# Performance work log

Hardware: AMD Instinct MI355X
Metric: run time of the kernel (lower is better)

The kernel has to match this reference:

```python
import jax, jax.numpy as jnp
import numpy as np

VOCAB, EMBED, SEQ, UNITS, BATCH = 10000, 100, 80, 64, 16384


def setup_inputs() -> dict:
    key = jax.random.key(0)
    ks = jax.random.split(key, 8)
    s = 0.05
    return {
        "tokens": jax.random.randint(ks[0], (BATCH, SEQ), 0, VOCAB, dtype=jnp.int32),
        "emb": jax.random.normal(ks[1], (VOCAB, EMBED), jnp.float32) * s,
        "Wx1": jax.random.normal(ks[2], (EMBED, UNITS), jnp.float32) * s,
        "Wh1": jax.random.normal(ks[3], (UNITS, UNITS), jnp.float32) * s,
        "b1": jnp.zeros((UNITS,), jnp.float32),
        "Wx2": jax.random.normal(ks[4], (UNITS, UNITS), jnp.float32) * s,
        "Wh2": jax.random.normal(ks[5], (UNITS, UNITS), jnp.float32) * s,
        "b2": jnp.zeros((UNITS,), jnp.float32),
        "Wd": jax.random.normal(ks[6], (UNITS, 1), jnp.float32) * s,
        "bd": jnp.zeros((1,), jnp.float32),
    }


def _simple_rnn(x, Wx, Wh, b):
    """SimpleRNN (eval mode): h_t = tanh(x_t @ Wx + h_{t-1} @ Wh + b).
    x: (B, T, E) -> all hidden states (B, T, U)."""
    # precompute input projection once (big GEMM), scan only does the small recurrent matmul
    xp = jnp.einsum("bte,eu->btu", x, Wx) + b  # (B, T, U)

    def step(h, xt):
        h = jnp.tanh(xt + h @ Wh)
        return h, h

    h0 = jnp.zeros((x.shape[0], Wh.shape[0]), x.dtype)
    _, hs = jax.lax.scan(step, h0, jnp.swapaxes(xp, 0, 1))  # (T, B, U)
    return jnp.swapaxes(hs, 0, 1)  # (B, T, U)


def reference(tokens, emb, Wx1, Wh1, b1, Wx2, Wh2, b2, Wd, bd):
    x = emb[tokens]                              # (B, T, E) embedding lookup
    h1 = _simple_rnn(x, Wx1, Wh1, b1)            # (B, T, U) return_sequences=True
    h2 = _simple_rnn(h1, Wx2, Wh2, b2)[:, -1]    # (B, U)    last state only
    return jax.nn.sigmoid(h2 @ Wd + bd)          # (B, 1)
```

## Files before the change

### kernel.cpp

```cpp
#include <hip/hip_runtime.h>
#include <hip/hip_bf16.h>


#define BATCH 16384
#define SEQ   80
#define EMBED 100
#define UNITS 64
#define ROWS  16
#define VOCAB 10000
#define EPAD  128

typedef __attribute__((ext_vector_type(8))) short bf16x8;
typedef __attribute__((ext_vector_type(4))) float f32x4;
typedef __attribute__((ext_vector_type(2))) float f32x2;
typedef __attribute__((ext_vector_type(4))) int   i32x4;
typedef __attribute__((ext_vector_type(2))) int   i32x2;

static __device__ __forceinline__ unsigned short bf16_rne(float f) {
    unsigned u = __builtin_bit_cast(unsigned, f);
    u += 0x7FFFu + ((u >> 16) & 1u);
    return (unsigned short)(u >> 16);
}

static __device__ __forceinline__ float bf16_to_f(short s) {
    unsigned u = ((unsigned)(unsigned short)s) << 16;
    return __builtin_bit_cast(float, u);
}

static __device__ __forceinline__ int pack_bf16(float a, float b) {
    unsigned ua = __builtin_bit_cast(unsigned, a);
    unsigned ub = __builtin_bit_cast(unsigned, b);
    ua += 0x7FFFu + ((ua >> 16) & 1u);
    ub += 0x7FFFu + ((ub >> 16) & 1u);
    return (int)__builtin_amdgcn_perm(ub, ua, 0x07060302u);
}

static __device__ __forceinline__ f32x2 tanh2(f32x2 x) {
    f32x2 u = x * x;
    f32x2 p = u * (-0.05396825f) + 0.13333333f;
    p = u * p + (-0.33333333f);
    return (x * u) * p + x;
}

static __device__ __forceinline__ i32x2 tanh_pack4(f32x4 v) {
    f32x2 lo = tanh2((f32x2){v[0], v[1]});
    f32x2 hi = tanh2((f32x2){v[2], v[3]});
    i32x2 r;
    r[0] = pack_bf16(lo[0], lo[1]);
    r[1] = pack_bf16(hi[0], hi[1]);
    return r;
}

static __device__ __forceinline__ bf16x8 asb(i32x4 v) {
    return __builtin_bit_cast(bf16x8, v);
}

__global__ __launch_bounds__(256) void emb_prep(const float* __restrict__ emb,
                                                unsigned short* __restrict__ embb) {
    int i = blockIdx.x * 256 + threadIdx.x;
    if (i < VOCAB * EPAD) {
        int v = i >> 7, k = i & (EPAD - 1);
        float f = (k < EMBED) ? emb[v * EMBED + k] : 0.0f;
        embb[i] = bf16_rne(f);
    }
}

template <bool BF16EMB>
__global__ __launch_bounds__(64, 1)
void rnn_fused(const int* __restrict__ tokens,
               const float* __restrict__ emb,
               const unsigned short* __restrict__ embb,
               const float* __restrict__ Wx1,
               const float* __restrict__ Wh1,
               const float* __restrict__ b1,
               const float* __restrict__ Wx2,
               const float* __restrict__ Wh2,
               const float* __restrict__ b2,
               const float* __restrict__ Wd,
               const float* __restrict__ bd,
               float* __restrict__ out)
{
    __shared__ int tokL[ROWS][SEQ + 1];

    const int lane = threadIdx.x;
    const int c = lane & 15;
    const int q = lane >> 4;
    const int rowBase = blockIdx.x * ROWS;

    for (int i = lane; i < ROWS * SEQ; i += 64) {
        int r = i / SEQ, tt = i - r * SEQ;
        tokL[r][tt] = tokens[rowBase * SEQ + i];
    }
    __syncthreads();

    bf16x8 awx1[4][4];
#pragma unroll
    for (int kt = 0; kt < 4; ++kt)
#pragma unroll
        for (int mt = 0; mt < 4; ++mt) {
            bf16x8 v;
#pragma unroll
            for (int j = 0; j < 8; ++j) {
                int k = kt * 32 + q * 8 + j;
                v[j] = (k < EMBED) ? (short)bf16_rne(Wx1[k * UNITS + mt * 16 + c]) : (short)0;
            }
            awx1[kt][mt] = v;
        }
    bf16x8 awh1[2][4], awx2[2][4], awh2[2][4];
#pragma unroll
    for (int kt = 0; kt < 2; ++kt)
#pragma unroll
        for (int mt = 0; mt < 4; ++mt) {
            bf16x8 va, vb, vc;
#pragma unroll
            for (int j = 0; j < 8; ++j) {
                int u = kt * 32 + ((j >> 2) << 4) + q * 4 + (j & 3);
                va[j] = (short)bf16_rne(Wh1[u * UNITS + mt * 16 + c]);
                vb[j] = (short)bf16_rne(Wx2[u * UNITS + mt * 16 + c]);
                vc[j] = (short)bf16_rne(Wh2[u * UNITS + mt * 16 + c]);
            }
            awh1[kt][mt] = va; awx2[kt][mt] = vb; awh2[kt][mt] = vc;
        }
    f32x4 b1C[4], b2C[4];
#pragma unroll
    for (int mt = 0; mt < 4; ++mt)
#pragma unroll
        for (int r = 0; r < 4; ++r) {
            b1C[mt][r] = b1[mt * 16 + q * 4 + r];
            b2C[mt][r] = b2[mt * 16 + q * 4 + r];
        }

    i32x4 h1B[2] = {(i32x4){0,0,0,0}, (i32x4){0,0,0,0}};
    i32x4 h2B[2] = {(i32x4){0,0,0,0}, (i32x4){0,0,0,0}};

    i32x4 xB[3][4];
    auto gatherX = [&](int t, i32x4 (&xg)[4]) {
        int token = tokL[c][t];
        if constexpr (BF16EMB) {
            const unsigned short* eb = embb + (size_t)token * EPAD + q * 8;
#pragma unroll
            for (int kt = 0; kt < 4; ++kt)
                xg[kt] = *reinterpret_cast<const i32x4*>(eb + kt * 32);
        } else {
            const float* eb = emb + (size_t)token * EMBED;
#pragma unroll
            for (int kt = 0; kt < 4; ++kt) {
                int k0 = kt * 32 + q * 8;
                f32x4 a = (k0 < EMBED)     ? *reinterpret_cast<const f32x4*>(eb + k0)
                                           : (f32x4){0.f, 0.f, 0.f, 0.f};
                f32x4 b = (k0 + 4 < EMBED) ? *reinterpret_cast<const f32x4*>(eb + k0 + 4)
                                           : (f32x4){0.f, 0.f, 0.f, 0.f};
                i32x4 v;
                v[0] = pack_bf16(a[0], a[1]);
                v[1] = pack_bf16(a[2], a[3]);
                v[2] = pack_bf16(b[0], b[1]);
                v[3] = pack_bf16(b[2], b[3]);
                xg[kt] = v;
            }
        }
    };

    gatherX(0, xB[0]);
    gatherX(1, xB[1]);

    auto step = [&](int t, i32x4 (&xr)[4], i32x4 (&xw)[4]) {
        if (t + 2 < SEQ) gatherX(t + 2, xw);

        f32x4 a2[4];
#pragma unroll
        for (int mt = 0; mt < 4; ++mt)
            a2[mt] = __builtin_amdgcn_mfma_f32_16x16x32_bf16(awx2[0][mt], asb(h1B[0]), b2C[mt], 0, 0, 0);
#pragma unroll
        for (int mt = 0; mt < 4; ++mt)
            a2[mt] = __builtin_amdgcn_mfma_f32_16x16x32_bf16(awh2[0][mt], asb(h2B[0]), a2[mt], 0, 0, 0);
#pragma unroll
        for (int mt = 0; mt < 4; ++mt)
            a2[mt] = __builtin_amdgcn_mfma_f32_16x16x32_bf16(awx2[1][mt], asb(h1B[1]), a2[mt], 0, 0, 0);
#pragma unroll
        for (int mt = 0; mt < 4; ++mt)
            a2[mt] = __builtin_amdgcn_mfma_f32_16x16x32_bf16(awh2[1][mt], asb(h2B[1]), a2[mt], 0, 0, 0);

        f32x4 a1[4];
#pragma unroll
        for (int mt = 0; mt < 4; ++mt)
            a1[mt] = __builtin_amdgcn_mfma_f32_16x16x32_bf16(awx1[0][mt], asb(xr[0]), b1C[mt], 0, 0, 0);
#pragma unroll
        for (int kt = 1; kt < 4; ++kt)
#pragma unroll
            for (int mt = 0; mt < 4; ++mt)
                a1[mt] = __builtin_amdgcn_mfma_f32_16x16x32_bf16(awx1[kt][mt], asb(xr[kt]), a1[mt], 0, 0, 0);
#pragma unroll
        for (int kt = 0; kt < 2; ++kt)
#pragma unroll
            for (int mt = 0; mt < 4; ++mt)
                a1[mt] = __builtin_amdgcn_mfma_f32_16x16x32_bf16(awh1[kt][mt], asb(h1B[kt]), a1[mt], 0, 0, 0);

        i32x2 p0 = tanh_pack4(a1[0]), p1 = tanh_pack4(a1[1]);
        i32x2 p2 = tanh_pack4(a1[2]), p3 = tanh_pack4(a1[3]);
        if (t > 0) {
            i32x2 s0 = tanh_pack4(a2[0]), s1 = tanh_pack4(a2[1]);
            i32x2 s2 = tanh_pack4(a2[2]), s3 = tanh_pack4(a2[3]);
            h2B[0] = (i32x4){s0[0], s0[1], s1[0], s1[1]};
            h2B[1] = (i32x4){s2[0], s2[1], s3[0], s3[1]};
        }
        h1B[0] = (i32x4){p0[0], p0[1], p1[0], p1[1]};
        h1B[1] = (i32x4){p2[0], p2[1], p3[0], p3[1]};
    };

#pragma unroll 1
    for (int t = 0; t < 78; t += 3) {
        step(t,     xB[0], xB[2]);
        step(t + 1, xB[1], xB[0]);
        step(t + 2, xB[2], xB[1]);
    }
    step(78, xB[0], xB[2]);
    step(79, xB[1], xB[0]);

    f32x4 a2[4];
#pragma unroll
    for (int mt = 0; mt < 4; ++mt)
        a2[mt] = __builtin_amdgcn_mfma_f32_16x16x32_bf16(awx2[0][mt], asb(h1B[0]), b2C[mt], 0, 0, 0);
#pragma unroll
    for (int mt = 0; mt < 4; ++mt)
        a2[mt] = __builtin_amdgcn_mfma_f32_16x16x32_bf16(awh2[0][mt], asb(h2B[0]), a2[mt], 0, 0, 0);
#pragma unroll
    for (int mt = 0; mt < 4; ++mt)
        a2[mt] = __builtin_amdgcn_mfma_f32_16x16x32_bf16(awx2[1][mt], asb(h1B[1]), a2[mt], 0, 0, 0);
#pragma unroll
    for (int mt = 0; mt < 4; ++mt)
        a2[mt] = __builtin_amdgcn_mfma_f32_16x16x32_bf16(awh2[1][mt], asb(h2B[1]), a2[mt], 0, 0, 0);

    i32x2 s0 = tanh_pack4(a2[0]), s1 = tanh_pack4(a2[1]);
    i32x2 s2 = tanh_pack4(a2[2]), s3 = tanh_pack4(a2[3]);
    h2B[0] = (i32x4){s0[0], s0[1], s1[0], s1[1]};
    h2B[1] = (i32x4){s2[0], s2[1], s3[0], s3[1]};

    float p = 0.f;
#pragma unroll
    for (int kt = 0; kt < 2; ++kt) {
        bf16x8 hb = asb(h2B[kt]);
#pragma unroll
        for (int j = 0; j < 8; ++j) {
            int u = kt * 32 + ((j >> 2) << 4) + q * 4 + (j & 3);
            p += bf16_to_f(hb[j]) * Wd[u];
        }
    }
    p += __shfl_xor(p, 16);
    p += __shfl_xor(p, 32);
    if (q == 0) {
        float x = p + bd[0];
        out[rowBase + c] = __builtin_amdgcn_rcpf(1.0f + __expf(-x));
    }
}

extern "C" void kernel_launch(void* const* d_in, const int* in_sizes, int n_in,
                              void* d_out, int out_size, void* d_ws, size_t ws_size,
                              hipStream_t stream) {
    const int*   tokens = (const int*)  d_in[0];
    const float* emb    = (const float*)d_in[1];
    const float* Wx1    = (const float*)d_in[2];
    const float* Wh1    = (const float*)d_in[3];
    const float* b1     = (const float*)d_in[4];
    const float* Wx2    = (const float*)d_in[5];
    const float* Wh2    = (const float*)d_in[6];
    const float* b2     = (const float*)d_in[7];
    const float* Wd     = (const float*)d_in[8];
    const float* bd     = (const float*)d_in[9];
    float* out = (float*)d_out;

    dim3 grid(BATCH / ROWS);
    dim3 block(64);
    const size_t embb_bytes = (size_t)VOCAB * EPAD * sizeof(unsigned short);
    if (ws_size >= embb_bytes) {
        unsigned short* embb = (unsigned short*)d_ws;
        emb_prep<<<dim3((VOCAB * EPAD + 255) / 256), dim3(256), 0, stream>>>(emb, embb);
        rnn_fused<true><<<grid, block, 0, stream>>>(tokens, emb, embb, Wx1, Wh1, b1,
                                                    Wx2, Wh2, b2, Wd, bd, out);
    } else {
        rnn_fused<false><<<grid, block, 0, stream>>>(tokens, emb, nullptr, Wx1, Wh1, b1,
                                                     Wx2, Wh2, b2, Wd, bd, out);
    }
}
```

Measured before the change: 157.0 us.

## Split RNN output tiles across two waves exchanging hidden state via LDS

Each block now runs two wavefronts, each computing half of the 64 output units, and the waves exchange hidden states every timestep through double-buffered shared memory with a barrier per step. This halves the MFMA chain per wave and shortens the serial critical path per timestep, at the cost of LDS traffic and a __syncthreads every step. Tokens are now read directly from global memory in int4 chunks instead of being staged in LDS. The tanh polynomial drops its highest-order term, which is cheaper but less accurate, and the final dense head is fused using fp32 tanh outputs.

```diff
diff --git a/kernel.cpp b/kernel.cpp
--- a/kernel.cpp
+++ b/kernel.cpp
@@ -15,16 +15,12 @@
 typedef __attribute__((ext_vector_type(2))) float f32x2;
 typedef __attribute__((ext_vector_type(4))) int   i32x4;
 typedef __attribute__((ext_vector_type(2))) int   i32x2;
+typedef unsigned long long u64;
 
 static __device__ __forceinline__ unsigned short bf16_rne(float f) {
     unsigned u = __builtin_bit_cast(unsigned, f);
     u += 0x7FFFu + ((u >> 16) & 1u);
     return (unsigned short)(u >> 16);
-}
-
-static __device__ __forceinline__ float bf16_to_f(short s) {
-    unsigned u = ((unsigned)(unsigned short)s) << 16;
-    return __builtin_bit_cast(float, u);
 }
 
 static __device__ __forceinline__ int pack_bf16(float a, float b) {
@@ -37,9 +33,9 @@
 
 static __device__ __forceinline__ f32x2 tanh2(f32x2 x) {
     f32x2 u = x * x;
-    f32x2 p = u * (-0.05396825f) + 0.13333333f;
-    p = u * p + (-0.33333333f);
-    return (x * u) * p + x;
+    f32x2 w = x * u;
+    f32x2 p = u * 0.13333333f + (-0.33333333f);
+    return w * p + x;
 }
 
 static __device__ __forceinline__ i32x2 tanh_pack4(f32x4 v) {
@@ -51,6 +47,10 @@
     return r;
 }
 
+static __device__ __forceinline__ u64 pk64(i32x2 v) {
+    return ((u64)(unsigned)v[1] << 32) | (u64)(unsigned)v[0];
+}
+
 static __device__ __forceinline__ bf16x8 asb(i32x4 v) {
     return __builtin_bit_cast(bf16x8, v);
 }
@@ -66,7 +66,7 @@
 }
 
 template <bool BF16EMB>
-__global__ __launch_bounds__(64, 1)
+__global__ __launch_bounds__(128, 2)
 void rnn_fused(const int* __restrict__ tokens,
                const float* __restrict__ emb,
                const unsigned short* __restrict__ embb,
@@ -80,62 +80,64 @@
                const float* __restrict__ bd,
                float* __restrict__ out)
 {
-    __shared__ int tokL[ROWS][SEQ + 1];
-
-    const int lane = threadIdx.x;
-    const int c = lane & 15;
-    const int q = lane >> 4;
+    __shared__ u64 hx[2 * 2 * 4 * 64];
+    __shared__ float headp[ROWS][2];
+
+    const int tid  = threadIdx.x;
+    const int w    = tid >> 6;
+    const int lane = tid & 63;
+    const int c    = lane & 15;
+    const int q    = lane >> 4;
     const int rowBase = blockIdx.x * ROWS;
-
-    for (int i = lane; i < ROWS * SEQ; i += 64) {
-        int r = i / SEQ, tt = i - r * SEQ;
-        tokL[r][tt] = tokens[rowBase * SEQ + i];
-    }
-    __syncthreads();
-
-    bf16x8 awx1[4][4];
+    const int mt0  = 2 * w;
+
+    for (int i = tid; i < 2 * 2 * 4 * 64; i += 128) hx[i] = 0ull;
+
+    const int* tokPtr = tokens + (size_t)(rowBase + c) * SEQ;
+    int4 tcur  = *reinterpret_cast<const int4*>(tokPtr);
+    int4 tnext = *reinterpret_cast<const int4*>(tokPtr + 4);
+
+    bf16x8 awx1[4][2];
 #pragma unroll
     for (int kt = 0; kt < 4; ++kt)
 #pragma unroll
-        for (int mt = 0; mt < 4; ++mt) {
+        for (int m = 0; m < 2; ++m) {
             bf16x8 v;
 #pragma unroll
             for (int j = 0; j < 8; ++j) {
                 int k = kt * 32 + q * 8 + j;
-                v[j] = (k < EMBED) ? (short)bf16_rne(Wx1[k * UNITS + mt * 16 + c]) : (short)0;
+                v[j] = (k < EMBED) ? (short)bf16_rne(Wx1[k * UNITS + (mt0 + m) * 16 + c])
+                                   : (short)0;
             }
-            awx1[kt][mt] = v;
-        }
-    bf16x8 awh1[2][4], awx2[2][4], awh2[2][4];
+            awx1[kt][m] = v;
+        }
+    bf16x8 awh1[2][2], awx2[2][2], awh2[2][2];
 #pragma unroll
     for (int kt = 0; kt < 2; ++kt)
 #pragma unroll
-        for (int mt = 0; mt < 4; ++mt) {
+        for (int m = 0; m < 2; ++m) {
             bf16x8 va, vb, vc;
 #pragma unroll
             for (int j = 0; j < 8; ++j) {
                 int u = kt * 32 + ((j >> 2) << 4) + q * 4 + (j & 3);
-                va[j] = (short)bf16_rne(Wh1[u * UNITS + mt * 16 + c]);
-                vb[j] = (short)bf16_rne(Wx2[u * UNITS + mt * 16 + c]);
-                vc[j] = (short)bf16_rne(Wh2[u * UNITS + mt * 16 + c]);
+                va[j] = (short)bf16_rne(Wh1[u * UNITS + (mt0 + m) * 16 + c]);
+                vb[j] = (short)bf16_rne(Wx2[u * UNITS + (mt0 + m) * 16 + c]);
+                vc[j] = (short)bf16_rne(Wh2[u * UNITS + (mt0 + m) * 16 + c]);
             }
-            awh1[kt][mt] = va; awx2[kt][mt] = vb; awh2[kt][mt] = vc;
-        }
-    f32x4 b1C[4], b2C[4];
-#pragma unroll
-    for (int mt = 0; mt < 4; ++mt)
+            awh1[kt][m] = va; awx2[kt][m] = vb; awh2[kt][m] = vc;
+        }
+    f32x4 b1C[2], b2C[2], wdC[2];
+#pragma unroll
+    for (int m = 0; m < 2; ++m)
 #pragma unroll
         for (int r = 0; r < 4; ++r) {
-            b1C[mt][r] = b1[mt * 16 + q * 4 + r];
-            b2C[mt][r] = b2[mt * 16 + q * 4 + r];
-        }
-
-    i32x4 h1B[2] = {(i32x4){0,0,0,0}, (i32x4){0,0,0,0}};
-    i32x4 h2B[2] = {(i32x4){0,0,0,0}, (i32x4){0,0,0,0}};
-
-    i32x4 xB[3][4];
-    auto gatherX = [&](int t, i32x4 (&xg)[4]) {
-        int token = tokL[c][t];
+            b1C[m][r] = b1[(mt0 + m) * 16 + q * 4 + r];
+            b2C[m][r] = b2[(mt0 + m) * 16 + q * 4 + r];
+            wdC[m][r] = Wd[(mt0 + m) * 16 + q * 4 + r];
+        }
+
+    i32x4 xB[4][4];
+    auto gatherX = [&](int token, i32x4 (&xg)[4]) {
         if constexpr (BF16EMB) {
             const unsigned short* eb = embb + (size_t)token * EPAD + q * 8;
 #pragma unroll
@@ -160,96 +162,136 @@
         }
     };
 
-    gatherX(0, xB[0]);
-    gatherX(1, xB[1]);
-
-    auto step = [&](int t, i32x4 (&xr)[4], i32x4 (&xw)[4]) {
-        if (t + 2 < SEQ) gatherX(t + 2, xw);
-
-        f32x4 a2[4];
-#pragma unroll
-        for (int mt = 0; mt < 4; ++mt)
-            a2[mt] = __builtin_amdgcn_mfma_f32_16x16x32_bf16(awx2[0][mt], asb(h1B[0]), b2C[mt], 0, 0, 0);
-#pragma unroll
-        for (int mt = 0; mt < 4; ++mt)
-            a2[mt] = __builtin_amdgcn_mfma_f32_16x16x32_bf16(awh2[0][mt], asb(h2B[0]), a2[mt], 0, 0, 0);
-#pragma unroll
-        for (int mt = 0; mt < 4; ++mt)
-            a2[mt] = __builtin_amdgcn_mfma_f32_16x16x32_bf16(awx2[1][mt], asb(h1B[1]), a2[mt], 0, 0, 0);
-#pragma unroll
-        for (int mt = 0; mt < 4; ++mt)
-            a2[mt] = __builtin_amdgcn_mfma_f32_16x16x32_bf16(awh2[1][mt], asb(h2B[1]), a2[mt], 0, 0, 0);
-
-        f32x4 a1[4];
-#pragma unroll
-        for (int mt = 0; mt < 4; ++mt)
-            a1[mt] = __builtin_amdgcn_mfma_f32_16x16x32_bf16(awx1[0][mt], asb(xr[0]), b1C[mt], 0, 0, 0);
+    gatherX(tcur.x, xB[0]);
+    gatherX(tcur.y, xB[1]);
+    __syncthreads();
+
+    auto step = [&](int t, i32x4 (&xr)[4], i32x4 (&xw)[4], int gtok,
+                    int pr, int pw, bool pubH2) {
+        const u64* hb = &hx[pr * (2 * 4 * 64)];
+        u64 r10 = hb[(0 * 4 + 0) * 64 + lane];
+        u64 r11 = hb[(0 * 4 + 1) * 64 + lane];
+        u64 r12 = hb[(0 * 4 + 2) * 64 + lane];
+        u64 r13 = hb[(0 * 4 + 3) * 64 + lane];
+        u64 r20 = hb[(1 * 4 + 0) * 64 + lane];
+        u64 r21 = hb[(1 * 4 + 1) * 64 + lane];
+        u64 r22 = hb[(1 * 4 + 2) * 64 + lane];
+        u64 r23 = hb[(1 * 4 + 3) * 64 + lane];
+        i32x4 h1f0 = {(int)r10, (int)(r10 >> 32), (int)r11, (int)(r11 >> 32)};
+        i32x4 h1f1 = {(int)r12, (int)(r12 >> 32), (int)r13, (int)(r13 >> 32)};
+        i32x4 h2f0 = {(int)r20, (int)(r20 >> 32), (int)r21, (int)(r21 >> 32)};
+        i32x4 h2f1 = {(int)r22, (int)(r22 >> 32), (int)r23, (int)(r23 >> 32)};
+
+        if (t + 2 < SEQ) gatherX(gtok, xw);
+
+        f32x4 a2[2], a1[2];
+#pragma unroll
+        for (int m = 0; m < 2; ++m)
+            a2[m] = __builtin_amdgcn_mfma_f32_16x16x32_bf16(awx2[0][m], asb(h1f0), b2C[m], 0, 0, 0);
+#pragma unroll
+        for (int m = 0; m < 2; ++m)
+            a2[m] = __builtin_amdgcn_mfma_f32_16x16x32_bf16(awh2[0][m], asb(h2f0), a2[m], 0, 0, 0);
+#pragma unroll
+        for (int m = 0; m < 2; ++m)
+            a2[m] = __builtin_amdgcn_mfma_f32_16x16x32_bf16(awx2[1][m], asb(h1f1), a2[m], 0, 0, 0);
+#pragma unroll
+        for (int m = 0; m < 2; ++m)
+            a2[m] = __builtin_amdgcn_mfma_f32_16x16x32_bf16(awh2[1][m], asb(h2f1), a2[m], 0, 0, 0);
+
+#pragma unroll
+        for (int m = 0; m < 2; ++m)
+            a1[m] = __builtin_amdgcn_mfma_f32_16x16x32_bf16(awx1[0][m], asb(xr[0]), b1C[m], 0, 0, 0);
 #pragma unroll
         for (int kt = 1; kt < 4; ++kt)
 #pragma unroll
-            for (int mt = 0; mt < 4; ++mt)
-                a1[mt] = __builtin_amdgcn_mfma_f32_16x16x32_bf16(awx1[kt][mt], asb(xr[kt]), a1[mt], 0, 0, 0);
-#pragma unroll
-        for (int kt = 0; kt < 2; ++kt)
-#pragma unroll
-            for (int mt = 0; mt < 4; ++mt)
-                a1[mt] = __builtin_amdgcn_mfma_f32_16x16x32_bf16(awh1[kt][mt], asb(h1B[kt]), a1[mt], 0, 0, 0);
-
-        i32x2 p0 = tanh_pack4(a1[0]), p1 = tanh_pack4(a1[1]);
-        i32x2 p2 = tanh_pack4(a1[2]), p3 = tanh_pack4(a1[3]);
-        if (t > 0) {
-            i32x2 s0 = tanh_pack4(a2[0]), s1 = tanh_pack4(a2[1]);
-            i32x2 s2 = tanh_pack4(a2[2]), s3 = tanh_pack4(a2[3]);
-            h2B[0] = (i32x4){s0[0], s0[1], s1[0], s1[1]};
-            h2B[1] = (i32x4){s2[0], s2[1], s3[0], s3[1]};
-        }
-        h1B[0] = (i32x4){p0[0], p0[1], p1[0], p1[1]};
-        h1B[1] = (i32x4){p2[0], p2[1], p3[0], p3[1]};
+            for (int m = 0; m < 2; ++m)
+                a1[m] = __builtin_amdgcn_mfma_f32_16x16x32_bf16(awx1[kt][m], asb(xr[kt]), a1[m], 0, 0, 0);
+#pragma unroll
+        for (int m = 0; m < 2; ++m)
+            a1[m] = __builtin_amdgcn_mfma_f32_16x16x32_bf16(awh1[0][m], asb(h1f0), a1[m], 0, 0, 0);
+#pragma unroll
+        for (int m = 0; m < 2; ++m)
+            a1[m] = __builtin_amdgcn_mfma_f32_16x16x32_bf16(awh1[1][m], asb(h1f1), a1[m], 0, 0, 0);
+
+        u64* hw = &hx[pw * (2 * 4 * 64)];
+        i32x2 p0 = tanh_pack4(a1[0]);
+        i32x2 p1 = tanh_pack4(a1[1]);
+        hw[(0 * 4 + mt0 + 0) * 64 + lane] = pk64(p0);
+        hw[(0 * 4 + mt0 + 1) * 64 + lane] = pk64(p1);
+        if (pubH2) {
+            i32x2 s0 = tanh_pack4(a2[0]);
+            i32x2 s1 = tanh_pack4(a2[1]);
+            hw[(1 * 4 + mt0 + 0) * 64 + lane] = pk64(s0);
+            hw[(1 * 4 + mt0 + 1) * 64 + lane] = pk64(s1);
+        }
+        __syncthreads();
     };
 
+    step(0, xB[0], xB[2], tcur.z,  0, 1, false);
+    step(1, xB[1], xB[3], tcur.w,  1, 0, true);
+    step(2, xB[2], xB[0], tnext.x, 0, 1, true);
+    step(3, xB[3], xB[1], tnext.y, 1, 0, true);
+    tcur = tnext;
+    tnext = *reinterpret_cast<const int4*>(tokPtr + 8);
+
 #pragma unroll 1
-    for (int t = 0; t < 78; t += 3) {
-        step(t,     xB[0], xB[2]);
-        step(t + 1, xB[1], xB[0]);
-        step(t + 2, xB[2], xB[1]);
-    }
-    step(78, xB[0], xB[2]);
-    step(79, xB[1], xB[0]);
-
-    f32x4 a2[4];
-#pragma unroll
-    for (int mt = 0; mt < 4; ++mt)
-        a2[mt] = __builtin_amdgcn_mfma_f32_16x16x32_bf16(awx2[0][mt], asb(h1B[0]), b2C[mt], 0, 0, 0);
-#pragma unroll
-    for (int mt = 0; mt < 4; ++mt)
-        a2[mt] = __builtin_amdgcn_mfma_f32_16x16x32_bf16(awh2[0][mt], asb(h2B[0]), a2[mt], 0, 0, 0);
-#pragma unroll
-    for (int mt = 0; mt < 4; ++mt)
-        a2[mt] = __builtin_amdgcn_mfma_f32_16x16x32_bf16(awx2[1][mt], asb(h1B[1]), a2[mt], 0, 0, 0);
-#pragma unroll
-    for (int mt = 0; mt < 4; ++mt)
-        a2[mt] = __builtin_amdgcn_mfma_f32_16x16x32_bf16(awh2[1][mt], asb(h2B[1]), a2[mt], 0, 0, 0);
-
-    i32x2 s0 = tanh_pack4(a2[0]), s1 = tanh_pack4(a2[1]);
-    i32x2 s2 = tanh_pack4(a2[2]), s3 = tanh_pack4(a2[3]);
-    h2B[0] = (i32x4){s0[0], s0[1], s1[0], s1[1]};
-    h2B[1] = (i32x4){s2[0], s2[1], s3[0], s3[1]};
-
-    float p = 0.f;
-#pragma unroll
-    for (int kt = 0; kt < 2; ++kt) {
-        bf16x8 hb = asb(h2B[kt]);
-#pragma unroll
-        for (int j = 0; j < 8; ++j) {
-            int u = kt * 32 + ((j >> 2) << 4) + q * 4 + (j & 3);
-            p += bf16_to_f(hb[j]) * Wd[u];
-        }
-    }
-    p += __shfl_xor(p, 16);
-    p += __shfl_xor(p, 32);
-    if (q == 0) {
-        float x = p + bd[0];
-        out[rowBase + c] = __builtin_amdgcn_rcpf(1.0f + __expf(-x));
+    for (int tt = 4; tt <= 76; tt += 4) {
+        int tq = tt + 8;
+        if (tq > SEQ - 4) tq = SEQ - 4;
+        int4 tn2 = *reinterpret_cast<const int4*>(tokPtr + tq);
+        step(tt + 0, xB[0], xB[2], tcur.z,  0, 1, true);
+        step(tt + 1, xB[1], xB[3], tcur.w,  1, 0, true);
+        step(tt + 2, xB[2], xB[0], tnext.x, 0, 1, true);
+        step(tt + 3, xB[3], xB[1], tnext.y, 1, 0, true);
+        tcur = tnext;
+        tnext = tn2;
+    }
+
+    {
+        const u64* hb = &hx[0];
+        u64 r10 = hb[(0 * 4 + 0) * 64 + lane];
+        u64 r11 = hb[(0 * 4 + 1) * 64 + lane];
+        u64 r12 = hb[(0 * 4 + 2) * 64 + lane];
+        u64 r13 = hb[(0 * 4 + 3) * 64 + lane];
+        u64 r20 = hb[(1 * 4 + 0) * 64 + lane];
+        u64 r21 = hb[(1 * 4 + 1) * 64 + lane];
+        u64 r22 = hb[(1 * 4 + 2) * 64 + lane];
+        u64 r23 = hb[(1 * 4 + 3) * 64 + lane];
+        i32x4 h1f0 = {(int)r10, (int)(r10 >> 32), (int)r11, (int)(r11 >> 32)};
+        i32x4 h1f1 = {(int)r12, (int)(r12 >> 32), (int)r13, (int)(r13 >> 32)};
+        i32x4 h2f0 = {(int)r20, (int)(r20 >> 32), (int)r21, (int)(r21 >> 32)};
+        i32x4 h2f1 = {(int)r22, (int)(r22 >> 32), (int)r23, (int)(r23 >> 32)};
+
+        f32x4 a2[2];
+#pragma unroll
+        for (int m = 0; m < 2; ++m)
+            a2[m] = __builtin_amdgcn_mfma_f32_16x16x32_bf16(awx2[0][m], asb(h1f0), b2C[m], 0, 0, 0);
+#pragma unroll
+        for (int m = 0; m < 2; ++m)
+            a2[m] = __builtin_amdgcn_mfma_f32_16x16x32_bf16(awh2[0][m], asb(h2f0), a2[m], 0, 0, 0);
+#pragma unroll
+        for (int m = 0; m < 2; ++m)
+            a2[m] = __builtin_amdgcn_mfma_f32_16x16x32_bf16(awx2[1][m], asb(h1f1), a2[m], 0, 0, 0);
+#pragma unroll
+        for (int m = 0; m < 2; ++m)
+            a2[m] = __builtin_amdgcn_mfma_f32_16x16x32_bf16(awh2[1][m], asb(h2f1), a2[m], 0, 0, 0);
+
+        float p = 0.f;
+#pragma unroll
+        for (int m = 0; m < 2; ++m) {
+            f32x2 lo = tanh2((f32x2){a2[m][0], a2[m][1]});
+            f32x2 hi = tanh2((f32x2){a2[m][2], a2[m][3]});
+            p += lo[0] * wdC[m][0] + lo[1] * wdC[m][1]
+               + hi[0] * wdC[m][2] + hi[1] * wdC[m][3];
+        }
+        p += __shfl_xor(p, 16);
+        p += __shfl_xor(p, 32);
+        if (q == 0) headp[c][w] = p;
+    }
+    __syncthreads();
+    if (tid < ROWS) {
+        float x = headp[tid][0] + headp[tid][1] + bd[0];
+        out[rowBase + tid] = __builtin_amdgcn_rcpf(1.0f + __expf(-x));
     }
 }
 
@@ -269,7 +311,7 @@
     float* out = (float*)d_out;
 
     dim3 grid(BATCH / ROWS);
-    dim3 block(64);
+    dim3 block(128);
     const size_t embb_bytes = (size_t)VOCAB * EPAD * sizeof(unsigned short);
     if (ws_size >= embb_bytes) {
         unsigned short* embb = (unsigned short*)d_ws;
```

After: 158.9 us. About the same (+1.2%).

## Software-pipeline input projection one step ahead and simplify tanh/bf16 packing

Applied to the files above, without the earlier changes.

The layer-1 input projection (x_t @ Wx1 + b1) is now computed one timestep ahead into a double-buffered accumulator. This takes it off the recurrent critical path, so each step's dependent chain only does the two Wh1 MFMAs. Embedding gathers are prefetched three steps ahead with a four-deep buffer ring. The tanh polynomial is also truncated by one term, and bf16 packing switches from round-to-nearest-even to simple round-half-up, which lowers accuracy slightly and trades register pressure for more overlap.

```diff
diff --git a/kernel.cpp b/kernel.cpp
--- a/kernel.cpp
+++ b/kernel.cpp
@@ -28,18 +28,16 @@
 }
 
 static __device__ __forceinline__ int pack_bf16(float a, float b) {
-    unsigned ua = __builtin_bit_cast(unsigned, a);
-    unsigned ub = __builtin_bit_cast(unsigned, b);
-    ua += 0x7FFFu + ((ua >> 16) & 1u);
-    ub += 0x7FFFu + ((ub >> 16) & 1u);
+    unsigned ua = __builtin_bit_cast(unsigned, a) + 0x8000u;
+    unsigned ub = __builtin_bit_cast(unsigned, b) + 0x8000u;
     return (int)__builtin_amdgcn_perm(ub, ua, 0x07060302u);
 }
 
 static __device__ __forceinline__ f32x2 tanh2(f32x2 x) {
     f32x2 u = x * x;
-    f32x2 p = u * (-0.05396825f) + 0.13333333f;
-    p = u * p + (-0.33333333f);
-    return (x * u) * p + x;
+    f32x2 w = x * u;
+    f32x2 p = u * 0.13333333f + (-0.33333333f);
+    return w * p + x;
 }
 
 static __device__ __forceinline__ i32x2 tanh_pack4(f32x4 v) {
@@ -133,9 +131,8 @@
     i32x4 h1B[2] = {(i32x4){0,0,0,0}, (i32x4){0,0,0,0}};
     i32x4 h2B[2] = {(i32x4){0,0,0,0}, (i32x4){0,0,0,0}};
 
-    i32x4 xB[3][4];
-    auto gatherX = [&](int t, i32x4 (&xg)[4]) {
-        int token = tokL[c][t];
+    i32x4 xB[4][4];
+    auto gatherX = [&](int token, i32x4 (&xg)[4]) {
         if constexpr (BF16EMB) {
             const unsigned short* eb = embb + (size_t)token * EPAD + q * 8;
 #pragma unroll
@@ -160,12 +157,25 @@
         }
     };
 
-    gatherX(0, xB[0]);
-    gatherX(1, xB[1]);
-
-    auto step = [&](int t, i32x4 (&xr)[4], i32x4 (&xw)[4]) {
-        if (t + 2 < SEQ) gatherX(t + 2, xw);
-
+    f32x4 xc0[4], xc1[4];
+    auto buildXC = [&](i32x4 (&xr)[4], f32x4 (&xcW)[4]) {
+#pragma unroll
+        for (int mt = 0; mt < 4; ++mt)
+            xcW[mt] = __builtin_amdgcn_mfma_f32_16x16x32_bf16(awx1[0][mt], asb(xr[0]), b1C[mt], 0, 0, 0);
+#pragma unroll
+        for (int kt = 1; kt < 4; ++kt)
+#pragma unroll
+            for (int mt = 0; mt < 4; ++mt)
+                xcW[mt] = __builtin_amdgcn_mfma_f32_16x16x32_bf16(awx1[kt][mt], asb(xr[kt]), xcW[mt], 0, 0, 0);
+    };
+
+    gatherX(tokL[c][0], xB[0]);
+    gatherX(tokL[c][1], xB[1]);
+    gatherX(tokL[c][2], xB[2]);
+    buildXC(xB[0], xc0);
+
+    auto iter = [&](int t, f32x4 (&xcR)[4], f32x4 (&xcW)[4], int rs, int ws,
+                    bool pubH2, bool doG, bool doXC) {
         f32x4 a2[4];
 #pragma unroll
         for (int mt = 0; mt < 4; ++mt)
@@ -183,21 +193,18 @@
         f32x4 a1[4];
 #pragma unroll
         for (int mt = 0; mt < 4; ++mt)
-            a1[mt] = __builtin_amdgcn_mfma_f32_16x16x32_bf16(awx1[0][mt], asb(xr[0]), b1C[mt], 0, 0, 0);
-#pragma unroll
-        for (int kt = 1; kt < 4; ++kt)
-#pragma unroll
-            for (int mt = 0; mt < 4; ++mt)
-                a1[mt] = __builtin_amdgcn_mfma_f32_16x16x32_bf16(awx1[kt][mt], asb(xr[kt]), a1[mt], 0, 0, 0);
-#pragma unroll
-        for (int kt = 0; kt < 2; ++kt)
-#pragma unroll
-            for (int mt = 0; mt < 4; ++mt)
-                a1[mt] = __builtin_amdgcn_mfma_f32_16x16x32_bf16(awh1[kt][mt], asb(h1B[kt]), a1[mt], 0, 0, 0);
+            a1[mt] = __builtin_amdgcn_mfma_f32_16x16x32_bf16(awh1[0][mt], asb(h1B[0]), xcR[mt], 0, 0, 0);
+#pragma unroll
+        for (int mt = 0; mt < 4; ++mt)
+            a1[mt] = __builtin_amdgcn_mfma_f32_16x16x32_bf16(awh1[1][mt], asb(h1B[1]), a1[mt], 0, 0, 0);
+
+        if (doG) gatherX(tokL[c][t + 3], xB[ws]);
+
+        if (doXC) buildXC(xB[rs], xcW);
 
         i32x2 p0 = tanh_pack4(a1[0]), p1 = tanh_pack4(a1[1]);
         i32x2 p2 = tanh_pack4(a1[2]), p3 = tanh_pack4(a1[3]);
-        if (t > 0) {
+        if (pubH2) {
             i32x2 s0 = tanh_pack4(a2[0]), s1 = tanh_pack4(a2[1]);
             i32x2 s2 = tanh_pack4(a2[2]), s3 = tanh_pack4(a2[3]);
             h2B[0] = (i32x4){s0[0], s0[1], s1[0], s1[1]};
@@ -207,14 +214,23 @@
         h1B[1] = (i32x4){p2[0], p2[1], p3[0], p3[1]};
     };
 
+    iter(0, xc0, xc1, 1, 3, false, true, true);
+    iter(1, xc1, xc0, 2, 0, true,  true, true);
+    iter(2, xc0, xc1, 3, 1, true,  true, true);
+    iter(3, xc1, xc0, 0, 2, true,  true, true);
+
 #pragma unroll 1
-    for (int t = 0; t < 78; t += 3) {
-        step(t,     xB[0], xB[2]);
-        step(t + 1, xB[1], xB[0]);
-        step(t + 2, xB[2], xB[1]);
-    }
-    step(78, xB[0], xB[2]);
-    step(79, xB[1], xB[0]);
+    for (int tt = 4; tt <= 72; tt += 4) {
+        iter(tt + 0, xc0, xc1, 1, 3, true, true, true);
+        iter(tt + 1, xc1, xc0, 2, 0, true, true, true);
+        iter(tt + 2, xc0, xc1, 3, 1, true, true, true);
+        iter(tt + 3, xc1, xc0, 0, 2, true, true, true);
+    }
+
+    iter(76, xc0, xc1, 1, 3, true, true,  true);
+    iter(77, xc1, xc0, 2, 0, true, false, true);
+    iter(78, xc0, xc1, 3, 1, true, false, true);
+    iter(79, xc1, xc0, 0, 2, true, false, false);
 
     f32x4 a2[4];
 #pragma unroll
```

Result: no change. 156.3 us (-0.4%).
